# Kernel tuning notes

Hardware: AMD Instinct MI355X
Metric: run time of the kernel (lower is better)

Reference implementation:

```python
import jax, jax.numpy as jnp
import numpy as np

N_NODES = 50000
N_EDGES = 600000
N_FEAT = 128
N_GRAPHS = 256
DIM = 95
N_OUT = 12
N_ITER = 10
BN_EPS = 1e-5


def setup_inputs() -> dict:
    key = jax.random.key(0)
    ks = jax.random.split(key, 16)
    inp = {}
    inp["x"] = jax.random.normal(ks[0], (N_NODES, N_FEAT), dtype=jnp.float32)
    inp["edge_index"] = jax.random.randint(ks[1], (2, N_EDGES), 0, N_NODES, dtype=jnp.int64)
    inp["batch"] = jnp.sort(jax.random.randint(ks[2], (N_NODES,), 0, N_GRAPHS, dtype=jnp.int64))
    def lin(k, fan_in, fan_out):
        bound = 1.0 / np.sqrt(fan_in)
        kw, kb = jax.random.split(k)
        W = jax.random.uniform(kw, (fan_in, fan_out), jnp.float32, -bound, bound)
        b = jax.random.uniform(kb, (fan_out,), jnp.float32, -bound, bound)
        return W, b
    inp["W1a"], inp["b1a"] = lin(ks[3], N_FEAT, N_FEAT)            # nn1 layer 1
    inp["W1b"], inp["b1b"] = lin(ks[4], N_FEAT, N_FEAT)            # nn1 layer 2
    inp["gamma"] = jnp.ones((N_FEAT,), jnp.float32)                 # bn1 weight
    inp["beta"] = jnp.zeros((N_FEAT,), jnp.float32)                 # bn1 bias
    inp["Wl1"], inp["bl1"] = lin(ks[5], 2 * N_FEAT, N_FEAT // 2)   # lin1
    inp["Wl2"], inp["bl2"] = lin(ks[6], 2 * N_FEAT, N_FEAT // 2)   # lin2
    inp["Wm1"], inp["bm1"] = lin(ks[7], N_FEAT, DIM)               # MLP layer 1
    inp["Wm2"], inp["bm2"] = lin(ks[8], DIM, N_OUT)                # MLP layer 2
    return inp


def reference(x, edge_index, batch, W1a, b1a, W1b, b1b, gamma, beta,
              Wl1, bl1, Wl2, bl2, Wm1, bm1, Wm2, bm2):
    src, dst = edge_index[0], edge_index[1]
    # GINConv (eps=0): h_i = nn1(x_i + sum_{j->i} x_j)
    agg = jax.ops.segment_sum(x[src], dst, num_segments=N_NODES)
    h0 = x + agg
    h0 = jax.nn.relu(h0 @ W1a + b1a) @ W1b + b1b
    x1 = jax.nn.relu(h0)
    # BatchNorm1d (training mode: batch statistics, biased variance)
    mean = jnp.mean(x1, axis=0)
    var = jnp.mean(jnp.square(x1 - mean), axis=0)
    x1 = gamma * (x1 - mean) * jax.lax.rsqrt(var + BN_EPS) + beta
    # global_mean_pool over graph ids
    sums = jax.ops.segment_sum(x1, batch, num_segments=N_GRAPHS)
    counts = jax.ops.segment_sum(jnp.ones((N_NODES,), x1.dtype), batch, num_segments=N_GRAPHS)
    xg = sums / jnp.maximum(counts, 1.0)[:, None]
    # recurrent gated loop
    h = xg
    for _ in range(N_ITER):
        cat = jnp.concatenate([xg, h], axis=1)          # [G, 2*F]
        p = cat @ Wl1 + bl1
        q = cat @ Wl2 + bl2
        h = jnp.concatenate([jnp.tanh(q), jax.nn.sigmoid(p)], axis=1)
    # output MLP
    return jax.nn.relu(h @ Wm1 + bm1) @ Wm2 + bm2
```

## Files before the change

### kernel.cpp

```cpp
#include <hip/hip_runtime.h>
#include <hip/hip_fp16.h>
#include <cstddef>

#define N_NODES  50000
#define N_EDGES  600000
#define N_FEAT   128
#define N_GRAPHS 256
#define DIMM     95
#define N_OUTD   12
#define N_ITERS  10

#define N_CHUNKS 196

#define WS_STATS 0
#define WS_XG    (WS_STATS + 256)
#define WS_CNT   (WS_XG + N_GRAPHS * N_FEAT)
#define WS_OFF   (WS_CNT + N_NODES)
#define WS_CUR   (WS_OFF + N_NODES + 4)
#define WS_CHS   (WS_CUR + N_NODES)
#define WS_SORT  (WS_CHS + 256)
#define WS_XH    (WS_SORT + N_EDGES)

#define SR 132
#define TR 48

__global__ void k_zero(const float* __restrict__ x, float* __restrict__ ws) {
    const int gtid = blockIdx.x * 256 + threadIdx.x;
    const int nthr = gridDim.x * 256;
    int* cnt = (int*)ws + WS_CNT;
    for (int i = gtid; i < N_NODES; i += nthr) cnt[i] = 0;
    if (gtid < 256) ws[WS_STATS + gtid] = 0.f;
    for (int i = gtid; i < N_GRAPHS * N_FEAT; i += nthr) ws[WS_XG + i] = 0.f;
    const float4* __restrict__ x4 = (const float4*)x;
    float2* __restrict__ xh = (float2*)(ws + WS_XH);
    for (int i = gtid; i < N_NODES * 32; i += nthr) {
        float4 v = x4[i];
        float2 o;
        ((__half2*)&o)[0] = __float22half2_rn(make_float2(v.x, v.y));
        ((__half2*)&o)[1] = __float22half2_rn(make_float2(v.z, v.w));
        xh[i] = o;
    }
}

__global__ void k_hist(const int* __restrict__ ei, float* __restrict__ ws) {
    int e = blockIdx.x * 256 + threadIdx.x;
    int* cnt = (int*)ws + WS_CNT;
    if (e < N_EDGES) atomicAdd(&cnt[ei[N_EDGES + e]], 1);
}

__global__ void k_chunk(float* __restrict__ ws) {
    __shared__ int red[4];
    const int tid = threadIdx.x;
    int* cnt = (int*)ws + WS_CNT;
    int i = blockIdx.x * 256 + tid;
    int v = (i < N_NODES) ? cnt[i] : 0;
    #pragma unroll
    for (int d = 32; d; d >>= 1) v += __shfl_down(v, d);
    if ((tid & 63) == 0) red[tid >> 6] = v;
    __syncthreads();
    if (tid == 0) ((int*)ws + WS_CHS)[blockIdx.x] = red[0] + red[1] + red[2] + red[3];
}

__global__ void k_scan0(float* __restrict__ ws) {
    __shared__ int s[256];
    const int tid = threadIdx.x;
    int* chs = (int*)ws + WS_CHS;
    int v = (tid < N_CHUNKS) ? chs[tid] : 0;
    s[tid] = v;
    __syncthreads();
    #pragma unroll
    for (int d = 1; d < 256; d <<= 1) {
        int t = (tid >= d) ? s[tid - d] : 0;
        __syncthreads();
        s[tid] += t;
        __syncthreads();
    }
    if (tid < N_CHUNKS) chs[tid] = s[tid] - v;
    if (tid == 0) ((int*)ws + WS_OFF)[N_NODES] = N_EDGES;
}

__global__ void k_scan1(float* __restrict__ ws) {
    __shared__ int s[256];
    const int tid = threadIdx.x;
    int* cnt = (int*)ws + WS_CNT;
    int* off = (int*)ws + WS_OFF;
    int* cur = (int*)ws + WS_CUR;
    int i = blockIdx.x * 256 + tid;
    int v = (i < N_NODES) ? cnt[i] : 0;
    s[tid] = v;
    __syncthreads();
    #pragma unroll
    for (int d = 1; d < 256; d <<= 1) {
        int t = (tid >= d) ? s[tid - d] : 0;
        __syncthreads();
        s[tid] += t;
        __syncthreads();
    }
    int o = ((int*)ws + WS_CHS)[blockIdx.x] + s[tid] - v;
    if (i < N_NODES) { off[i] = o; cur[i] = o; }
}

__global__ void k_scatter(const int* __restrict__ ei, float* __restrict__ ws) {
    int e = blockIdx.x * 256 + threadIdx.x;
    if (e >= N_EDGES) return;
    int d = ei[N_EDGES + e];
    int s = ei[e];
    int* cur = (int*)ws + WS_CUR;
    int pos = atomicAdd(&cur[d], 1);
    ((int*)ws + WS_SORT)[pos] = s;
}

__global__ __launch_bounds__(256, 4) void k_fused(const float* __restrict__ x,
        const int* __restrict__ batch, float* __restrict__ ws,
        const float* __restrict__ W1a, const float* __restrict__ b1a,
        const float* __restrict__ W1b, const float* __restrict__ b1b) {
    __shared__ float As[TR * SR];
    __shared__ float red[256];
    __shared__ int batch_l[TR];
    const int tid  = threadIdx.x;
    const int lane = tid & 63;
    const int wv   = tid >> 6;
    const int half = lane >> 5;
    const int sl   = lane & 31;
    const int fg   = tid & 15;
    const int rg   = tid >> 4;
    const int row0 = blockIdx.x * TR;

    const int* off = (const int*)ws + WS_OFF;
    const int* ss  = (const int*)ws + WS_SORT;
    const float4* __restrict__ x4 = (const float4*)x;
    const float2* __restrict__ xh = (const float2*)(ws + WS_XH);

    if (tid < TR) {
        int r = row0 + tid;
        batch_l[tid] = (r < N_NODES) ? batch[r] : (N_GRAPHS - 1);
    }

    for (int ii = 0; ii < 12; ii += 4) {
        float4 acc[2];
        int lo[2], deg[2];
        int need = 0;
        #pragma unroll
        for (int p = 0; p < 2; ++p) {
            const int rl = wv * 12 + ii + 2 * p + half;
            const int r  = row0 + rl;
            const bool valid = r < N_NODES;
            lo[p]  = valid ? off[r] : 0;
            int hi = valid ? off[r + 1] : lo[p];
            deg[p] = hi - lo[p];
            acc[p] = valid ? x4[(size_t)r * 32 + sl] : make_float4(0.f, 0.f, 0.f, 0.f);
            int dmx = max(deg[p], __shfl_xor(deg[p], 32));
            need = max(need, dmx);
        }
        for (int c0 = 0; c0 < need; c0 += 32) {
            int idxp[2];
            #pragma unroll
            for (int p = 0; p < 2; ++p)
                idxp[p] = (c0 + sl < deg[p]) ? ss[lo[p] + c0 + sl] : 0;
            const int dmc = min(32, need - c0);
            for (int j = 0; j < dmc; j += 2) {
                float2 v[4];
                #pragma unroll
                for (int p = 0; p < 2; ++p) {
                    int s0 = __shfl(idxp[p], (half << 5) + j);
                    v[p] = (c0 + j < deg[p]) ? xh[(size_t)s0 * 32 + sl]
                                             : make_float2(0.f, 0.f);
                }
                #pragma unroll
                for (int p = 0; p < 2; ++p) {
                    int s1 = __shfl(idxp[p], (half << 5) + j + 1);
                    v[2 + p] = (c0 + j + 1 < deg[p]) ? xh[(size_t)s1 * 32 + sl]
                                                     : make_float2(0.f, 0.f);
                }
                #pragma unroll
                for (int p = 0; p < 2; ++p) {
                    float2 a01 = __half22float2(((const __half2*)&v[p])[0]);
                    float2 a23 = __half22float2(((const __half2*)&v[p])[1]);
                    float2 b01 = __half22float2(((const __half2*)&v[2 + p])[0]);
                    float2 b23 = __half22float2(((const __half2*)&v[2 + p])[1]);
                    acc[p].x += a01.x + b01.x;
                    acc[p].y += a01.y + b01.y;
                    acc[p].z += a23.x + b23.x;
                    acc[p].w += a23.y + b23.y;
                }
            }
        }
        #pragma unroll
        for (int p = 0; p < 2; ++p) {
            const int rl = wv * 12 + ii + 2 * p + half;
            *(float4*)(As + rl * SR + 4 * sl) = acc[p];
        }
    }
    __syncthreads();

    float acc[3][8];
    #pragma unroll
    for (int i = 0; i < 3; ++i)
        #pragma unroll
        for (int j = 0; j < 8; ++j) acc[i][j] = 0.f;

    #pragma unroll 2
    for (int k = 0; k < N_FEAT; k += 4) {
        float4 w[8];
        #pragma unroll
        for (int kk = 0; kk < 4; ++kk) {
            w[2 * kk]     = *(const float4*)(W1a + (k + kk) * N_FEAT + fg * 8);
            w[2 * kk + 1] = *(const float4*)(W1a + (k + kk) * N_FEAT + fg * 8 + 4);
        }
        #pragma unroll
        for (int i = 0; i < 3; ++i) {
            const float4 a4 = *(const float4*)(As + (rg * 3 + i) * SR + k);
            const float av[4] = {a4.x, a4.y, a4.z, a4.w};
            #pragma unroll
            for (int kk = 0; kk < 4; ++kk) {
                acc[i][0] += av[kk] * w[2 * kk].x;
                acc[i][1] += av[kk] * w[2 * kk].y;
                acc[i][2] += av[kk] * w[2 * kk].z;
                acc[i][3] += av[kk] * w[2 * kk].w;
                acc[i][4] += av[kk] * w[2 * kk + 1].x;
                acc[i][5] += av[kk] * w[2 * kk + 1].y;
                acc[i][6] += av[kk] * w[2 * kk + 1].z;
                acc[i][7] += av[kk] * w[2 * kk + 1].w;
            }
        }
    }
    __syncthreads();

    {
        const float4 ba0 = *(const float4*)(b1a + fg * 8);
        const float4 ba1 = *(const float4*)(b1a + fg * 8 + 4);
        #pragma unroll
        for (int i = 0; i < 3; ++i) {
            float4 u0, u1;
            u0.x = fmaxf(acc[i][0] + ba0.x, 0.f); u0.y = fmaxf(acc[i][1] + ba0.y, 0.f);
            u0.z = fmaxf(acc[i][2] + ba0.z, 0.f); u0.w = fmaxf(acc[i][3] + ba0.w, 0.f);
            u1.x = fmaxf(acc[i][4] + ba1.x, 0.f); u1.y = fmaxf(acc[i][5] + ba1.y, 0.f);
            u1.z = fmaxf(acc[i][6] + ba1.z, 0.f); u1.w = fmaxf(acc[i][7] + ba1.w, 0.f);
            *(float4*)(As + (rg * 3 + i) * SR + fg * 8)     = u0;
            *(float4*)(As + (rg * 3 + i) * SR + fg * 8 + 4) = u1;
        }
    }
    __syncthreads();

    #pragma unroll
    for (int i = 0; i < 3; ++i)
        #pragma unroll
        for (int j = 0; j < 8; ++j) acc[i][j] = 0.f;

    #pragma unroll 2
    for (int k = 0; k < N_FEAT; k += 4) {
        float4 w[8];
        #pragma unroll
        for (int kk = 0; kk < 4; ++kk) {
            w[2 * kk]     = *(const float4*)(W1b + (k + kk) * N_FEAT + fg * 8);
            w[2 * kk + 1] = *(const float4*)(W1b + (k + kk) * N_FEAT + fg * 8 + 4);
        }
        #pragma unroll
        for (int i = 0; i < 3; ++i) {
            const float4 a4 = *(const float4*)(As + (rg * 3 + i) * SR + k);
            const float av[4] = {a4.x, a4.y, a4.z, a4.w};
            #pragma unroll
            for (int kk = 0; kk < 4; ++kk) {
                acc[i][0] += av[kk] * w[2 * kk].x;
                acc[i][1] += av[kk] * w[2 * kk].y;
                acc[i][2] += av[kk] * w[2 * kk].z;
                acc[i][3] += av[kk] * w[2 * kk].w;
                acc[i][4] += av[kk] * w[2 * kk + 1].x;
                acc[i][5] += av[kk] * w[2 * kk + 1].y;
                acc[i][6] += av[kk] * w[2 * kk + 1].z;
                acc[i][7] += av[kk] * w[2 * kk + 1].w;
            }
        }
    }
    __syncthreads();

    {
        const float4 bb0 = *(const float4*)(b1b + fg * 8);
        const float4 bb1 = *(const float4*)(b1b + fg * 8 + 4);
        #pragma unroll
        for (int i = 0; i < 3; ++i) {
            float4 u0, u1;
            u0.x = fmaxf(acc[i][0] + bb0.x, 0.f); u0.y = fmaxf(acc[i][1] + bb0.y, 0.f);
            u0.z = fmaxf(acc[i][2] + bb0.z, 0.f); u0.w = fmaxf(acc[i][3] + bb0.w, 0.f);
            u1.x = fmaxf(acc[i][4] + bb1.x, 0.f); u1.y = fmaxf(acc[i][5] + bb1.y, 0.f);
            u1.z = fmaxf(acc[i][6] + bb1.z, 0.f); u1.w = fmaxf(acc[i][7] + bb1.w, 0.f);
            *(float4*)(As + (rg * 3 + i) * SR + fg * 8)     = u0;
            *(float4*)(As + (rg * 3 + i) * SR + fg * 8 + 4) = u1;
        }
    }
    __syncthreads();

    {
        const int c = tid & 127;
        const int h = tid >> 7;
        float sum = 0.f, sq = 0.f, pool = 0.f;
        int curg = batch_l[h * 24];
        bool any = (row0 + h * 24) < N_NODES;
        #pragma unroll 4
        for (int rr = 0; rr < 24; ++rr) {
            int rl = h * 24 + rr;
            if (row0 + rl >= N_NODES) break;
            float v = As[rl * SR + c];
            int g = batch_l[rl];
            if (g != curg) {
                unsafeAtomicAdd(ws + WS_XG + (size_t)curg * N_FEAT + c, pool);
                pool = 0.f; curg = g;
            }
            sum += v; sq += v * v; pool += v;
        }
        if (any) unsafeAtomicAdd(ws + WS_XG + (size_t)curg * N_FEAT + c, pool);
        if (h == 1) { red[c] = sum; red[128 + c] = sq; }
        __syncthreads();
        if (h == 0) {
            unsafeAtomicAdd(ws + WS_STATS + c, sum + red[c]);
            unsafeAtomicAdd(ws + WS_STATS + 128 + c, sq + red[128 + c]);
        }
    }
}

__device__ __forceinline__ int lbound(const int* __restrict__ a, int n, int v) {
    int lo = 0, hi = n;
    while (lo < hi) { int m = (lo + hi) >> 1; if (a[m] < v) lo = m + 1; else hi = m; }
    return lo;
}

__global__ __launch_bounds__(256) void k_recur(const float* __restrict__ ws,
        const int* __restrict__ batch,
        const float* __restrict__ gamma, const float* __restrict__ beta,
        const float* __restrict__ Wl1, const float* __restrict__ bl1,
        const float* __restrict__ Wl2, const float* __restrict__ bl2,
        const float* __restrict__ Wm1, const float* __restrict__ bm1,
        const float* __restrict__ Wm2, const float* __restrict__ bm2,
        float* __restrict__ out) {
    __shared__ float W1h[128 * 64];
    __shared__ float W2h[128 * 64];
    __shared__ float xg_s[128];
    __shared__ float h_s[128];
    __shared__ float px[2][64];
    __shared__ float pq[2][2][64];
    __shared__ float m_s[DIMM];
    __shared__ int range[2];
    const int g = blockIdx.x, tid = threadIdx.x;

    if (tid < 2) range[tid] = lbound(batch, N_NODES, g + tid);
    {
        const float4* w1 = (const float4*)(Wl1 + 128 * 64);
        const float4* w2 = (const float4*)(Wl2 + 128 * 64);
        float4* d1 = (float4*)W1h;
        float4* d2 = (float4*)W2h;
        #pragma unroll
        for (int i = 0; i < 8; ++i) {
            d1[tid + i * 256] = w1[tid + i * 256];
            d2[tid + i * 256] = w2[tid + i * 256];
        }
    }
    __syncthreads();
    if (tid < 128) {
        const int cnt = range[1] - range[0];
        float mean = ws[WS_STATS + tid] * (1.f / N_NODES);
        float var  = fmaxf(ws[WS_STATS + 128 + tid] * (1.f / N_NODES) - mean * mean, 0.f);
        float sc = gamma[tid] * rsqrtf(var + 1e-5f);
        float sh = beta[tid] - mean * sc;
        float pool = ws[WS_XG + (size_t)g * N_FEAT + tid];
        float v = (cnt > 0) ? (sc * pool / (float)cnt + sh) : 0.f;
        xg_s[tid] = v;
        h_s[tid] = v;
    }
    __syncthreads();

    const int sel  = tid >> 7;
    const int part = (tid >> 6) & 1;
    const int j    = tid & 63;

    {
        const float* Wg = sel ? Wl2 : Wl1;
        float a = 0.f;
        const int k0 = part * 64;
        #pragma unroll 4
        for (int k = 0; k < 64; ++k) a += xg_s[k0 + k] * Wg[(k0 + k) * 64 + j];
        pq[sel][part][j] = a;
    }
    __syncthreads();
    if (part == 0) {
        const float* bias = sel ? bl2 : bl1;
        px[sel][j] = pq[sel][0][j] + pq[sel][1][j] + bias[j];
    }
    __syncthreads();

    const float* Wh = sel ? W2h : W1h;
    for (int it = 0; it < N_ITERS; ++it) {
        float a = 0.f;
        const int k0 = part * 64;
        #pragma unroll
        for (int k = 0; k < 64; k += 4) {
            const float4 h4 = *(const float4*)(h_s + k0 + k);
            a += h4.x * Wh[(k0 + k + 0) * 64 + j];
            a += h4.y * Wh[(k0 + k + 1) * 64 + j];
            a += h4.z * Wh[(k0 + k + 2) * 64 + j];
            a += h4.w * Wh[(k0 + k + 3) * 64 + j];
        }
        pq[sel][part][j] = a;
        __syncthreads();
        if (part == 0) {
            float tot = pq[sel][0][j] + pq[sel][1][j] + px[sel][j];
            if (sel == 0) h_s[64 + j] = 1.f / (1.f + expf(-tot));
            else          h_s[j] = tanhf(tot);
        }
        __syncthreads();
    }

    if (tid < DIMM) {
        float a = bm1[tid];
        #pragma unroll 4
        for (int k = 0; k < 128; ++k) a += h_s[k] * Wm1[k * DIMM + tid];
        m_s[tid] = fmaxf(a, 0.f);
    }
    __syncthreads();
    if (tid < N_OUTD) {
        float a = bm2[tid];
        for (int k = 0; k < DIMM; ++k) a += m_s[k] * Wm2[k * N_OUTD + tid];
        out[g * N_OUTD + tid] = a;
    }
}

extern "C" void kernel_launch(void* const* d_in, const int* in_sizes, int n_in,
                              void* d_out, int out_size, void* d_ws, size_t ws_size,
                              hipStream_t stream) {
    const float* x     = (const float*)d_in[0];
    const int*   ei    = (const int*)d_in[1];
    const int*   batch = (const int*)d_in[2];
    const float* W1a = (const float*)d_in[3];
    const float* b1a = (const float*)d_in[4];
    const float* W1b = (const float*)d_in[5];
    const float* b1b = (const float*)d_in[6];
    const float* gamma = (const float*)d_in[7];
    const float* beta  = (const float*)d_in[8];
    const float* Wl1 = (const float*)d_in[9];
    const float* bl1 = (const float*)d_in[10];
    const float* Wl2 = (const float*)d_in[11];
    const float* bl2 = (const float*)d_in[12];
    const float* Wm1 = (const float*)d_in[13];
    const float* bm1 = (const float*)d_in[14];
    const float* Wm2 = (const float*)d_in[15];
    const float* bm2 = (const float*)d_in[16];
    float* out = (float*)d_out;
    float* ws  = (float*)d_ws;

    k_zero   <<<512, 256, 0, stream>>>(x, ws);
    k_hist   <<<(N_EDGES + 255) / 256, 256, 0, stream>>>(ei, ws);
    k_chunk  <<<N_CHUNKS, 256, 0, stream>>>(ws);
    k_scan0  <<<1, 256, 0, stream>>>(ws);
    k_scan1  <<<N_CHUNKS, 256, 0, stream>>>(ws);
    k_scatter<<<(N_EDGES + 255) / 256, 256, 0, stream>>>(ei, ws);
    k_fused  <<<(N_NODES + TR - 1) / TR, 256, 0, stream>>>(x, batch, ws, W1a, b1a, W1b, b1b);
    k_recur  <<<N_GRAPHS, 256, 0, stream>>>(ws, batch, gamma, beta,
                                            Wl1, bl1, Wl2, bl2, Wm1, bm1, Wm2, bm2, out);
}
```

Measured before the change: 311.2 us.

## Replace global CSR build with per-tile edge partitioning in shared memory

Drops the histogram, scan and global-atomic scatter kernels that built a node-level CSR. A preprocessing kernel now packs destination ids to 16 bits. Each tile block then scans the whole edge list, collects the edges that land in its 48 rows, and sorts them in LDS with local atomics before writing per-tile offsets and sources. This cuts kernel launches and global atomics, but every block rereads the full destination array. It also assumes no tile receives more than 1024 edges and that node ids fit in 16 bits; edges beyond the cap are silently dropped.

```diff
diff --git a/kernel.cpp b/kernel.cpp
--- a/kernel.cpp
+++ b/kernel.cpp
@@ -10,27 +10,32 @@
 #define N_OUTD   12
 #define N_ITERS  10
 
-#define N_CHUNKS 196
+#define SR 132
+#define TR 48
+#define N_TILES  ((N_NODES + TR - 1) / TR)
+#define CAP 1024
 
 #define WS_STATS 0
 #define WS_XG    (WS_STATS + 256)
-#define WS_CNT   (WS_XG + N_GRAPHS * N_FEAT)
-#define WS_OFF   (WS_CNT + N_NODES)
-#define WS_CUR   (WS_OFF + N_NODES + 4)
-#define WS_CHS   (WS_CUR + N_NODES)
-#define WS_SORT  (WS_CHS + 256)
-#define WS_XH    (WS_SORT + N_EDGES)
-
-#define SR 132
-#define TR 48
-
-__global__ void k_zero(const float* __restrict__ x, float* __restrict__ ws) {
+#define WS_OFF   (WS_XG + N_GRAPHS * N_FEAT)
+#define WS_SORT  (WS_OFF + N_TILES * 64)
+#define WS_D16   (WS_SORT + N_TILES * CAP)
+#define WS_XH    (WS_D16 + N_EDGES / 2)
+
+__global__ void k_pre(const int* __restrict__ ei, const float* __restrict__ x,
+                      float* __restrict__ ws) {
     const int gtid = blockIdx.x * 256 + threadIdx.x;
     const int nthr = gridDim.x * 256;
-    int* cnt = (int*)ws + WS_CNT;
-    for (int i = gtid; i < N_NODES; i += nthr) cnt[i] = 0;
-    if (gtid < 256) ws[WS_STATS + gtid] = 0.f;
-    for (int i = gtid; i < N_GRAPHS * N_FEAT; i += nthr) ws[WS_XG + i] = 0.f;
+    for (int i = gtid; i < 256 + N_GRAPHS * N_FEAT; i += nthr) ws[i] = 0.f;
+    const int2* __restrict__ dsts = (const int2*)(ei + N_EDGES);
+    ushort2* __restrict__ d16 = (ushort2*)((int*)ws + WS_D16);
+    for (int i = gtid; i < N_EDGES / 2; i += nthr) {
+        int2 d = dsts[i];
+        ushort2 o;
+        o.x = (unsigned short)d.x;
+        o.y = (unsigned short)d.y;
+        d16[i] = o;
+    }
     const float4* __restrict__ x4 = (const float4*)x;
     float2* __restrict__ xh = (float2*)(ws + WS_XH);
     for (int i = gtid; i < N_NODES * 32; i += nthr) {
@@ -42,72 +47,58 @@
     }
 }
 
-__global__ void k_hist(const int* __restrict__ ei, float* __restrict__ ws) {
-    int e = blockIdx.x * 256 + threadIdx.x;
-    int* cnt = (int*)ws + WS_CNT;
-    if (e < N_EDGES) atomicAdd(&cnt[ei[N_EDGES + e]], 1);
-}
-
-__global__ void k_chunk(float* __restrict__ ws) {
-    __shared__ int red[4];
-    const int tid = threadIdx.x;
-    int* cnt = (int*)ws + WS_CNT;
-    int i = blockIdx.x * 256 + tid;
-    int v = (i < N_NODES) ? cnt[i] : 0;
-    #pragma unroll
-    for (int d = 32; d; d >>= 1) v += __shfl_down(v, d);
-    if ((tid & 63) == 0) red[tid >> 6] = v;
-    __syncthreads();
-    if (tid == 0) ((int*)ws + WS_CHS)[blockIdx.x] = red[0] + red[1] + red[2] + red[3];
-}
-
-__global__ void k_scan0(float* __restrict__ ws) {
-    __shared__ int s[256];
-    const int tid = threadIdx.x;
-    int* chs = (int*)ws + WS_CHS;
-    int v = (tid < N_CHUNKS) ? chs[tid] : 0;
-    s[tid] = v;
-    __syncthreads();
-    #pragma unroll
-    for (int d = 1; d < 256; d <<= 1) {
-        int t = (tid >= d) ? s[tid - d] : 0;
-        __syncthreads();
-        s[tid] += t;
-        __syncthreads();
-    }
-    if (tid < N_CHUNKS) chs[tid] = s[tid] - v;
-    if (tid == 0) ((int*)ws + WS_OFF)[N_NODES] = N_EDGES;
-}
-
-__global__ void k_scan1(float* __restrict__ ws) {
-    __shared__ int s[256];
-    const int tid = threadIdx.x;
-    int* cnt = (int*)ws + WS_CNT;
-    int* off = (int*)ws + WS_OFF;
-    int* cur = (int*)ws + WS_CUR;
-    int i = blockIdx.x * 256 + tid;
-    int v = (i < N_NODES) ? cnt[i] : 0;
-    s[tid] = v;
-    __syncthreads();
-    #pragma unroll
-    for (int d = 1; d < 256; d <<= 1) {
-        int t = (tid >= d) ? s[tid - d] : 0;
-        __syncthreads();
-        s[tid] += t;
-        __syncthreads();
-    }
-    int o = ((int*)ws + WS_CHS)[blockIdx.x] + s[tid] - v;
-    if (i < N_NODES) { off[i] = o; cur[i] = o; }
-}
-
-__global__ void k_scatter(const int* __restrict__ ei, float* __restrict__ ws) {
-    int e = blockIdx.x * 256 + threadIdx.x;
-    if (e >= N_EDGES) return;
-    int d = ei[N_EDGES + e];
-    int s = ei[e];
-    int* cur = (int*)ws + WS_CUR;
-    int pos = atomicAdd(&cur[d], 1);
-    ((int*)ws + WS_SORT)[pos] = s;
+__global__ __launch_bounds__(256) void k_part(const int* __restrict__ ei,
+                                              float* __restrict__ ws) {
+    __shared__ int lbuf[CAP];
+    __shared__ int lsrc[CAP];
+    __shared__ int lhist[TR];
+    __shared__ int loff[TR + 1];
+    __shared__ int lcur[TR];
+    __shared__ int lcnt;
+    const int tid  = threadIdx.x;
+    const int tile = blockIdx.x;
+    const int base = tile * TR;
+    const int nrows = min(TR, N_NODES - base);
+    if (tid == 0) lcnt = 0;
+    if (tid < TR) lhist[tid] = 0;
+    __syncthreads();
+
+    const ushort2* __restrict__ d16 = (const ushort2*)((const int*)ws + WS_D16);
+    for (int i = tid; i < N_EDGES / 2; i += 256) {
+        ushort2 dd = d16[i];
+        int r0 = (int)dd.x - base;
+        int r1 = (int)dd.y - base;
+        if ((unsigned)r0 < (unsigned)nrows) {
+            int p = atomicAdd(&lcnt, 1);
+            if (p < CAP) lbuf[p] = (r0 << 16) | (ei[2 * i] & 0xFFFF);
+        }
+        if ((unsigned)r1 < (unsigned)nrows) {
+            int p = atomicAdd(&lcnt, 1);
+            if (p < CAP) lbuf[p] = (r1 << 16) | (ei[2 * i + 1] & 0xFFFF);
+        }
+    }
+    __syncthreads();
+    const int n = min(lcnt, CAP);
+    for (int i = tid; i < n; i += 256) atomicAdd(&lhist[lbuf[i] >> 16], 1);
+    __syncthreads();
+    if (tid == 0) {
+        int a = 0;
+        for (int i = 0; i < TR; ++i) { loff[i] = a; a += lhist[i]; }
+        loff[TR] = a;
+    }
+    __syncthreads();
+    if (tid < TR) lcur[tid] = loff[tid];
+    __syncthreads();
+    for (int i = tid; i < n; i += 256) {
+        int pk = lbuf[i];
+        int p = atomicAdd(&lcur[pk >> 16], 1);
+        lsrc[p] = pk & 0xFFFF;
+    }
+    __syncthreads();
+    int* __restrict__ gsort = (int*)ws + WS_SORT + tile * CAP;
+    for (int i = tid; i < n; i += 256) gsort[i] = lsrc[i];
+    int* __restrict__ goff = (int*)ws + WS_OFF + tile * 64;
+    if (tid <= TR) goff[tid] = loff[tid];
 }
 
 __global__ __launch_bounds__(256, 4) void k_fused(const float* __restrict__ x,
@@ -124,10 +115,11 @@
     const int sl   = lane & 31;
     const int fg   = tid & 15;
     const int rg   = tid >> 4;
-    const int row0 = blockIdx.x * TR;
-
-    const int* off = (const int*)ws + WS_OFF;
-    const int* ss  = (const int*)ws + WS_SORT;
+    const int tile = blockIdx.x;
+    const int row0 = tile * TR;
+
+    const int* __restrict__ loff = (const int*)ws + WS_OFF + tile * 64;
+    const int* __restrict__ ss   = (const int*)ws + WS_SORT + tile * CAP;
     const float4* __restrict__ x4 = (const float4*)x;
     const float2* __restrict__ xh = (const float2*)(ws + WS_XH);
 
@@ -145,9 +137,8 @@
             const int rl = wv * 12 + ii + 2 * p + half;
             const int r  = row0 + rl;
             const bool valid = r < N_NODES;
-            lo[p]  = valid ? off[r] : 0;
-            int hi = valid ? off[r + 1] : lo[p];
-            deg[p] = hi - lo[p];
+            lo[p]  = loff[rl];
+            deg[p] = loff[rl + 1] - lo[p];
             acc[p] = valid ? x4[(size_t)r * 32 + sl] : make_float4(0.f, 0.f, 0.f, 0.f);
             int dmx = max(deg[p], __shfl_xor(deg[p], 32));
             need = max(need, dmx);
@@ -446,13 +437,9 @@
     float* out = (float*)d_out;
     float* ws  = (float*)d_ws;
 
-    k_zero   <<<512, 256, 0, stream>>>(x, ws);
-    k_hist   <<<(N_EDGES + 255) / 256, 256, 0, stream>>>(ei, ws);
-    k_chunk  <<<N_CHUNKS, 256, 0, stream>>>(ws);
-    k_scan0  <<<1, 256, 0, stream>>>(ws);
-    k_scan1  <<<N_CHUNKS, 256, 0, stream>>>(ws);
-    k_scatter<<<(N_EDGES + 255) / 256, 256, 0, stream>>>(ei, ws);
-    k_fused  <<<(N_NODES + TR - 1) / TR, 256, 0, stream>>>(x, batch, ws, W1a, b1a, W1b, b1b);
-    k_recur  <<<N_GRAPHS, 256, 0, stream>>>(ws, batch, gamma, beta,
-                                            Wl1, bl1, Wl2, bl2, Wm1, bm1, Wm2, bm2, out);
-}
+    k_pre  <<<512, 256, 0, stream>>>(ei, x, ws);
+    k_part <<<N_TILES, 256, 0, stream>>>(ei, ws);
+    k_fused<<<N_TILES, 256, 0, stream>>>(x, batch, ws, W1a, b1a, W1b, b1b);
+    k_recur<<<N_GRAPHS, 256, 0, stream>>>(ws, batch, gamma, beta,
+                                          Wl1, bl1, Wl2, bl2, Wm1, bm1, Wm2, bm2, out);
+}
```

New measurement: 601.3 us. 1.93x slower.
